# Kernel tuning notes

Measured on AMD Instinct MI355X. Metric: run time of the kernel, lower is better.

Reference implementation:

```python
import jax, jax.numpy as jnp
import numpy as np

# dims: batch, time, d_model, d_state, experts, top-k, expert hidden, regime, layers
B, T, D, S, E, K, H, R, L = 4, 512, 384, 32, 6, 2, 512, 5, 2
DI = 2 * D          # d_inner = expand * d_model
DTR = D // 16       # dt_rank = 24


def setup_inputs() -> dict:
    key = jax.random.key(0)
    ks = iter(jax.random.split(key, 48))
    def nrm(shape, s=0.02):
        return jax.random.normal(next(ks), shape, jnp.float32) * s
    inp = {}
    inp["x"] = jax.random.normal(next(ks), (B, T, D), jnp.float32)
    r = jax.random.uniform(next(ks), (B, R), jnp.float32)
    inp["regime"] = r / r.sum(-1, keepdims=True)  # regime posterior
    # FiLM conditioner
    inp["film_w1"] = nrm((R, D)); inp["film_b1"] = jnp.zeros((D,), jnp.float32)
    inp["film_w2"] = nrm((D, 2 * D)); inp["film_b2"] = jnp.zeros((2 * D,), jnp.float32)
    # SelectiveSSMBlock params, stacked over L layers
    inp["ssm_ng"] = jnp.ones((L, D), jnp.float32); inp["ssm_nb"] = jnp.zeros((L, D), jnp.float32)
    inp["in_w"] = nrm((L, D, 2 * DI))
    inp["xp_w"] = nrm((L, DI, DTR + 2 * S))
    inp["dt_w"] = nrm((L, DTR, DI)); inp["dt_b"] = jnp.zeros((L, DI), jnp.float32)
    inp["a_log_real"] = jnp.log(jnp.clip(-0.5 * jax.random.normal(next(ks), (L, DI, S), jnp.float32), 1e-4, None))
    inp["a_imag"] = 0.1 * jax.random.normal(next(ks), (L, DI, S), jnp.float32)
    inp["ssm_d"] = jnp.ones((L, DI), jnp.float32)
    inp["out_w"] = nrm((L, DI, D))
    # MoELayer params, stacked over L layers
    inp["moe_ng"] = jnp.ones((L, D), jnp.float32); inp["moe_nb"] = jnp.zeros((L, D), jnp.float32)
    inp["r_w1"] = nrm((L, D + R, D)); inp["r_b1"] = jnp.zeros((L, D), jnp.float32)
    inp["r_w2"] = nrm((L, D, E)); inp["r_b2"] = jnp.zeros((L, E), jnp.float32)
    inp["e_w1"] = nrm((L, E, D, H)); inp["e_b1"] = jnp.zeros((L, E, H), jnp.float32)
    inp["e_w2"] = nrm((L, E, H, D)); inp["e_b2"] = jnp.zeros((L, E, D), jnp.float32)
    # final norm
    inp["fin_g"] = jnp.ones((D,), jnp.float32); inp["fin_b"] = jnp.zeros((D,), jnp.float32)
    return inp


def _ln(x, g, b):
    m = x.mean(-1, keepdims=True)
    v = ((x - m) ** 2).mean(-1, keepdims=True)
    return (x - m) * jax.lax.rsqrt(v + 1e-5) * g + b


def _ssm_block(h, ng, nb, in_w, xp_w, dt_w, dt_b, alr, aim, d_vec, out_w):
    B_, T_, _ = h.shape
    xn = _ln(h, ng, nb)
    xz = xn @ in_w                        # (B,T,2*DI)
    x_ssm, z = xz[..., :DI], xz[..., DI:]
    x_dbl = x_ssm @ xp_w                  # (B,T,DTR+2S)
    dt = jax.nn.softplus(x_dbl[..., :DTR] @ dt_w + dt_b)   # (B,T,DI)
    Bp = x_dbl[..., DTR:DTR + S]          # (B,T,S)
    Cp = x_dbl[..., DTR + S:]             # (B,T,S)
    A = (-jnp.exp(alr) + 1j * aim).astype(jnp.complex64)   # (DI,S)

    def step(hc, inp):
        dt_t, bt, ct, xt = inp            # (B,DI),(B,S),(B,S),(B,DI)
        dA = jnp.exp(A[None] * dt_t[:, :, None])                       # (B,DI,S) complex
        hc = dA * hc + ((dt_t * xt)[:, :, None] * bt[:, None, :]).astype(jnp.complex64)
        # (h*C).sum(-1).real == (h.real*C).sum(-1) since C is real
        y = jnp.einsum('bds,bs->bd', hc.real, ct)
        return hc, y

    h0 = jnp.zeros((B_, DI, S), jnp.complex64)
    xsT = (jnp.moveaxis(dt, 1, 0), jnp.moveaxis(Bp, 1, 0),
           jnp.moveaxis(Cp, 1, 0), jnp.moveaxis(x_ssm, 1, 0))
    _, ysT = jax.lax.scan(step, h0, xsT)
    y = jnp.moveaxis(ysT, 0, 1) + d_vec * x_ssm   # skip term D*x
    y = y * jax.nn.silu(z)
    return h + y @ out_w                  # residual (dropout=0)


def _moe(h, regime, ng, nb, rw1, rb1, rw2, rb2, ew1, eb1, ew2, eb2):
    xn = _ln(h, ng, nb)
    B_, T_, _ = xn.shape
    reg = jnp.broadcast_to(regime[:, None, :], (B_, T_, R))
    ri = jnp.concatenate([xn, reg], -1)
    gl = jax.nn.silu(ri @ rw1 + rb1) @ rw2 + rb2    # (B,T,E)
    tv, ti = jax.lax.top_k(gl, K)
    tw = jax.nn.softmax(tv, -1)
    eo = jax.nn.silu(jnp.einsum('btd,edh->bteh', xn, ew1) + eb1)
    eo = jnp.einsum('bteh,ehd->bted', eo, ew2) + eb2   # (B,T,E,D)
    sel = jnp.take_along_axis(eo, ti[..., None], axis=2)  # (B,T,K,D)
    out = (sel * tw[..., None]).sum(2)
    gp = jax.nn.softmax(gl, -1)
    avg_p = gp.mean((0, 1))
    avg_m = jax.nn.one_hot(ti[..., 0], E, dtype=gl.dtype).mean((0, 1))
    aux = 0.01 * E * (avg_p * avg_m).sum()
    return h + out, aux


def reference(x, regime, film_w1, film_b1, film_w2, film_b2, ssm_ng, ssm_nb, in_w,
              xp_w, dt_w, dt_b, a_log_real, a_imag, ssm_d, out_w, moe_ng, moe_nb,
              r_w1, r_b1, r_w2, r_b2, e_w1, e_b1, e_w2, e_b2, fin_g, fin_b):
    # FiLM conditioning from regime posterior
    gb = jax.nn.silu(regime @ film_w1 + film_b1) @ film_w2 + film_b2
    gamma, beta = gb[:, :D], gb[:, D:]
    h = x * (gamma[:, None, :] + 1.0) + beta[:, None, :]
    aux = jnp.float32(0.0)
    for l in range(L):
        h = _ssm_block(h, ssm_ng[l], ssm_nb[l], in_w[l], xp_w[l], dt_w[l], dt_b[l],
                       a_log_real[l], a_imag[l], ssm_d[l], out_w[l])
        h, a = _moe(h, regime, moe_ng[l], moe_nb[l], r_w1[l], r_b1[l], r_w2[l], r_b2[l],
                    e_w1[l], e_b1[l], e_w2[l], e_b2[l])
        aux = aux + a
    out = _ln(h, fin_g, fin_b)
    return out, aux
```

## Files before the change

### kernel.cpp

```cpp
#include <hip/hip_runtime.h>
#include <hip/hip_bf16.h>
#include <math.h>

#define B_   4
#define T_   512
#define D_   384
#define S_   32
#define E_   6
#define H_   512
#define R_   5
#define L_   2
#define DI_  768
#define DTR_ 24
#define BT_  2048
#define XPN_ 88
#define SCH  64
#define PIT  40
#define SPD  12
#define SPB  66

typedef short s8v __attribute__((ext_vector_type(8)));
typedef float f32x4 __attribute__((ext_vector_type(4)));
typedef ushort u16x8 __attribute__((ext_vector_type(8)));

__device__ __forceinline__ float siluf(float x) { return x / (1.f + __expf(-x)); }
__device__ __forceinline__ ushort f2b(float f) {
    unsigned u = __float_as_uint(f);
    return (ushort)((u + 0x7FFFu + ((u >> 16) & 1u)) >> 16);
}
__device__ __forceinline__ float b2f(ushort h) { return __uint_as_float(((unsigned)h) << 16); }

#define CN0 1179648L
#define CN1 135168L
#define CN2 36864L
#define CN3 589824L
#define CN4 2359296L
#define CN5 2359296L
#define CN6 294912L
__global__ void conv_k(const float* __restrict__ in_w, const float* __restrict__ xp_w,
                       const float* __restrict__ dt_w, const float* __restrict__ out_w,
                       const float* __restrict__ e_w1, const float* __restrict__ e_w2,
                       const float* __restrict__ r_w1,
                       ushort* __restrict__ in_wb, ushort* __restrict__ xp_wb,
                       ushort* __restrict__ dt_wb, ushort* __restrict__ out_wb,
                       ushort* __restrict__ e1b, ushort* __restrict__ e2b,
                       ushort* __restrict__ r1h, ushort* __restrict__ r1l)
{
    const long total = CN0 + CN1 + CN2 + CN3 + CN4 + CN5 + CN6;
    long stride = (long)gridDim.x * 256;
    for (long i = (long)blockIdx.x * 256 + threadIdx.x; i < total; i += stride) {
        long j = i;
        if (j < CN0) { in_wb[j] = f2b(in_w[j]); continue; }
        j -= CN0;
        if (j < CN1) { xp_wb[j] = f2b(xp_w[j]); continue; }
        j -= CN1;
        if (j < CN2) { dt_wb[j] = f2b(dt_w[j]); continue; }
        j -= CN2;
        if (j < CN3) { out_wb[j] = f2b(out_w[j]); continue; }
        j -= CN3;
        if (j < CN4) { e1b[j] = f2b(e_w1[j]); continue; }
        j -= CN4;
        if (j < CN5) { e2b[j] = f2b(e_w2[j]); continue; }
        j -= CN5;
        {
            long l = j / 147456, rem = j - l * 147456;
            float v = r_w1[l * (long)((D_ + R_) * D_) + rem];
            ushort hv = f2b(v);
            r1h[j] = hv;
            r1l[j] = f2b(v - b2f(hv));
        }
    }
}

__global__ void film_k(const float* __restrict__ regime, const float* __restrict__ w1,
                       const float* __restrict__ b1, const float* __restrict__ w2,
                       const float* __restrict__ b2, float* __restrict__ gb,
                       float* __restrict__ stats)
{
    int b = blockIdx.x;
    int tid = threadIdx.x;
    if (b == 0 && tid < 40) stats[tid] = 0.f;
    __shared__ float t1[D_];
    if (tid < D_) {
        float a = b1[tid];
        for (int r = 0; r < R_; r++) a += regime[b * R_ + r] * w1[r * D_ + tid];
        t1[tid] = siluf(a);
    }
    __syncthreads();
    float a = b2[tid];
    for (int d = 0; d < D_; d++) a += t1[d] * w2[d * (2 * D_) + tid];
    gb[b * (2 * D_) + tid] = a;
}

__global__ void film_apply_k(const float* __restrict__ x, const float* __restrict__ gb,
                             float* __restrict__ h)
{
    int i = blockIdx.x * 256 + threadIdx.x;
    if (i >= B_ * T_ * D_) return;
    int b = i / (T_ * D_);
    int d = i % D_;
    h[i] = x[i] * (1.f + gb[b * (2 * D_) + d]) + gb[b * (2 * D_) + D_ + d];
}

template<int MODE>
__global__ __launch_bounds__(256) void ln_k(const float* __restrict__ in,
                                            const float* __restrict__ g, const float* __restrict__ b,
                                            float* __restrict__ outF,
                                            ushort* __restrict__ outH, ushort* __restrict__ outL)
{
    int row = blockIdx.x;
    int tid = threadIdx.x;
    const float* x = in + (size_t)row * D_;
    float v0 = x[tid];
    float v1 = (tid < D_ - 256) ? x[256 + tid] : 0.f;
    float s = v0 + v1, ss = v0 * v0 + v1 * v1;
#pragma unroll
    for (int o = 32; o > 0; o >>= 1) { s += __shfl_xor(s, o); ss += __shfl_xor(ss, o); }
    __shared__ float sb[8];
    int w = tid >> 6;
    if ((tid & 63) == 0) { sb[w] = s; sb[4 + w] = ss; }
    __syncthreads();
    s = sb[0] + sb[1] + sb[2] + sb[3];
    ss = sb[4] + sb[5] + sb[6] + sb[7];
    float mean = s * (1.f / D_);
    float var = ss * (1.f / D_) - mean * mean;
    float rstd = rsqrtf(var + 1e-5f);
#pragma unroll
    for (int p = 0; p < 2; p++) {
        int c = tid + p * 256;
        if (c >= D_) break;
        float v = (p ? v1 : v0);
        float o = (v - mean) * rstd * g[c] + b[c];
        size_t idx = (size_t)row * D_ + c;
        if (MODE == 0) outF[idx] = o;
        else {
            ushort hv = f2b(o);
            outH[idx] = hv;
            if (MODE == 2) outL[idx] = f2b(o - b2f(hv));
        }
    }
}

template<int MODE>
__global__ __launch_bounds__(256) void selln_k(float* __restrict__ h,
                                               const ushort* __restrict__ eodb,
                                               const float* __restrict__ tw,
                                               const int* __restrict__ tpos,
                                               const float* __restrict__ g, const float* __restrict__ b,
                                               float* __restrict__ outF,
                                               ushort* __restrict__ outH, ushort* __restrict__ outL)
{
    int row = blockIdx.x;
    int tid = threadIdx.x;
    float* hp = h + (size_t)row * D_;
    int p0 = tpos[row * 2], p1 = tpos[row * 2 + 1];
    float w0 = tw[row * 2], w1 = tw[row * 2 + 1];
    const ushort* e0 = eodb + (size_t)p0 * D_;
    const ushort* e1 = eodb + (size_t)p1 * D_;
    float v0 = hp[tid] + w0 * b2f(e0[tid]) + w1 * b2f(e1[tid]);
    float v1 = 0.f;
    if (tid < D_ - 256) v1 = hp[256 + tid] + w0 * b2f(e0[256 + tid]) + w1 * b2f(e1[256 + tid]);
    hp[tid] = v0;
    if (tid < D_ - 256) hp[256 + tid] = v1;
    float s = v0 + v1, ss = v0 * v0 + v1 * v1;
#pragma unroll
    for (int o = 32; o > 0; o >>= 1) { s += __shfl_xor(s, o); ss += __shfl_xor(ss, o); }
    __shared__ float sb[8];
    int w = tid >> 6;
    if ((tid & 63) == 0) { sb[w] = s; sb[4 + w] = ss; }
    __syncthreads();
    s = sb[0] + sb[1] + sb[2] + sb[3];
    ss = sb[4] + sb[5] + sb[6] + sb[7];
    float mean = s * (1.f / D_);
    float var = ss * (1.f / D_) - mean * mean;
    float rstd = rsqrtf(var + 1e-5f);
#pragma unroll
    for (int p = 0; p < 2; p++) {
        int c = tid + p * 256;
        if (c >= D_) break;
        float v = (p ? v1 : v0);
        float o = (v - mean) * rstd * g[c] + b[c];
        size_t idx = (size_t)row * D_ + c;
        if (MODE == 0) outF[idx] = o;
        else {
            ushort hv = f2b(o);
            outH[idx] = hv;
            if (MODE == 2) outL[idx] = f2b(o - b2f(hv));
        }
    }
}

template<int OM, bool NG, bool KG, bool GATHER>
__global__ __launch_bounds__(256) void gemm_b(
    const ushort* __restrict__ A, int lda, long aOff,
    const ushort* __restrict__ W, int ldw, long wOff,
    float* __restrict__ C, int ldc, long cOff,
    ushort* __restrict__ Cb, int ldcb, long cbOff, int nb16,
    const float* __restrict__ bias, long bOff,
    const int* __restrict__ glist, const int* __restrict__ gcnt,
    int N, int K, int act, int acc)
{
    __shared__ __align__(16) ushort As[2][64 * PIT];
    __shared__ __align__(16) ushort Bs[2][64 * PIT];
    const int z = blockIdx.z;
    const int bm = blockIdx.y * 64, bn = blockIdx.x * 64;
    int cnt = 0;
    if (gcnt) { cnt = gcnt[z]; if (bm >= cnt) return; }
    const int tid = threadIdx.x, w = tid >> 6, lane = tid & 63;
    const int wm = (w >> 1) * 32, wn = (w & 1) * 32;
    const int l16 = lane & 15, lk = lane >> 4;
    const int r0 = tid >> 2, c0 = (tid & 3) * 8;
    const ushort* Ab;
    if (GATHER) {
        int gr = bm + r0;
        int t_idx = (gr < cnt) ? glist[(size_t)z * BT_ + gr] : 0;
        Ab = A + (size_t)t_idx * lda;
    } else {
        Ab = A + (size_t)z * aOff + (size_t)(bm + r0) * lda;
    }
    const ushort* Wb = W + (size_t)z * wOff;

    f32x4 accv[2][2];
#pragma unroll
    for (int i = 0; i < 2; i++)
#pragma unroll
        for (int j = 0; j < 2; j++) accv[i][j] = (f32x4)0.f;

    u16x8 arg;
    ushort wrg[8];
    auto LOADA = [&](int k0) {
        arg = *reinterpret_cast<const u16x8*>(Ab + k0 + c0);
    };
    auto LOADW = [&](int k0) {
#pragma unroll
        for (int i = 0; i < 8; i++) {
            int kk = k0 + w * 8 + i;
            bool ok = (!KG || kk < K) && (!NG || (bn + lane) < N);
            wrg[i] = ok ? Wb[(size_t)kk * ldw + bn + lane] : (ushort)0;
        }
    };
    auto STORE = [&](int buf) {
        *reinterpret_cast<u16x8*>(&As[buf][r0 * PIT + c0]) = arg;
        *reinterpret_cast<ushort4*>(&Bs[buf][lane * PIT + w * 8]) =
            make_ushort4(wrg[0], wrg[1], wrg[2], wrg[3]);
        *reinterpret_cast<ushort4*>(&Bs[buf][lane * PIT + w * 8 + 4]) =
            make_ushort4(wrg[4], wrg[5], wrg[6], wrg[7]);
    };

    LOADA(0); LOADW(0); STORE(0);
    __syncthreads();
    const int NIT = (K + 31) / 32;
    for (int it = 0; it < NIT; it++) {
        int cur = it & 1;
        bool more = (it + 1 < NIT);
        if (more) { LOADA((it + 1) * 32); LOADW((it + 1) * 32); }
        s8v af[2], bfr[2];
#pragma unroll
        for (int mf = 0; mf < 2; mf++)
            af[mf] = *reinterpret_cast<const s8v*>(&As[cur][(wm + mf * 16 + l16) * PIT + lk * 8]);
#pragma unroll
        for (int nf = 0; nf < 2; nf++)
            bfr[nf] = *reinterpret_cast<const s8v*>(&Bs[cur][(wn + nf * 16 + l16) * PIT + lk * 8]);
#pragma unroll
        for (int mf = 0; mf < 2; mf++)
#pragma unroll
            for (int nf = 0; nf < 2; nf++)
                accv[mf][nf] = __builtin_amdgcn_mfma_f32_16x16x32_bf16(af[mf], bfr[nf], accv[mf][nf], 0, 0, 0);
        if (more) { STORE(cur ^ 1); __syncthreads(); }
    }

    const float* biasb = bias ? bias + (size_t)z * bOff : nullptr;
#pragma unroll
    for (int mf = 0; mf < 2; mf++) {
#pragma unroll
        for (int nf = 0; nf < 2; nf++) {
            int col = bn + wn + nf * 16 + l16;
            if (NG && col >= N) continue;
#pragma unroll
            for (int r = 0; r < 4; r++) {
                int rr = bm + wm + mf * 16 + lk * 4 + r;
                if (gcnt && rr >= cnt) continue;
                float v = accv[mf][nf][r];
                if (biasb) v += biasb[col];
                if (act == 1) v = siluf(v);
                else if (act == 2) v = (v > 0.f) ? v + log1pf(__expf(-v)) : log1pf(__expf(v));
                if (OM == 0 || OM == 2) {
                    float* Cz = C + (size_t)z * cOff;
                    size_t ci = (size_t)rr * ldc + col;
                    Cz[ci] = acc ? (Cz[ci] + v) : v;
                }
                if (OM == 1 || OM == 2) {
                    if (col < nb16)
                        (Cb + (size_t)z * cbOff)[(size_t)rr * ldcb + col] = f2b(v);
                }
                if (OM == 3) {
                    if (col < nb16)
                        Cb[(size_t)rr * ldcb + col] = f2b(v);
                    if (col >= 24) {
                        int q = col - 24;
                        C[(size_t)rr * 64 + ((q < 32) ? (2 * q) : (2 * (q - 32) + 1))] = v;
                    }
                }
            }
        }
    }
}

__global__ __launch_bounds__(256) void gemm3_k(
    const ushort* __restrict__ Ah, const ushort* __restrict__ Al, int lda,
    const ushort* __restrict__ Wh, const ushort* __restrict__ Wl, int ldw,
    const float* __restrict__ bias,
    const float* __restrict__ regime, const float* __restrict__ rw1t,
    const float* __restrict__ rw2l,
    float* __restrict__ glp,
    int K)
{
    __shared__ __align__(16) ushort sAh[64 * PIT], sAl[64 * PIT];
    __shared__ __align__(16) ushort sWh[64 * PIT], sWl[64 * PIT];
    __shared__ __align__(16) float sV[64 * 66];
    const int bm = blockIdx.y * 64, bn = blockIdx.x * 64;
    const int tid = threadIdx.x, w = tid >> 6, lane = tid & 63;
    const int wm = (w >> 1) * 32, wn = (w & 1) * 32;
    const int l16 = lane & 15, lk = lane >> 4;
    const int r0 = tid >> 2, c0 = (tid & 3) * 8;
    f32x4 accv[2][2];
#pragma unroll
    for (int i = 0; i < 2; i++)
#pragma unroll
        for (int j = 0; j < 2; j++) accv[i][j] = (f32x4)0.f;

    for (int k0 = 0; k0 < K; k0 += 32) {
        *reinterpret_cast<u16x8*>(&sAh[r0 * PIT + c0]) =
            *reinterpret_cast<const u16x8*>(Ah + (size_t)(bm + r0) * lda + k0 + c0);
        *reinterpret_cast<u16x8*>(&sAl[r0 * PIT + c0]) =
            *reinterpret_cast<const u16x8*>(Al + (size_t)(bm + r0) * lda + k0 + c0);
        {
            ushort th[8], tl[8];
#pragma unroll
            for (int i = 0; i < 8; i++) {
                int kk = k0 + w * 8 + i;
                th[i] = Wh[(size_t)kk * ldw + bn + lane];
                tl[i] = Wl[(size_t)kk * ldw + bn + lane];
            }
            *reinterpret_cast<ushort4*>(&sWh[lane * PIT + w * 8])     = make_ushort4(th[0], th[1], th[2], th[3]);
            *reinterpret_cast<ushort4*>(&sWh[lane * PIT + w * 8 + 4]) = make_ushort4(th[4], th[5], th[6], th[7]);
            *reinterpret_cast<ushort4*>(&sWl[lane * PIT + w * 8])     = make_ushort4(tl[0], tl[1], tl[2], tl[3]);
            *reinterpret_cast<ushort4*>(&sWl[lane * PIT + w * 8 + 4]) = make_ushort4(tl[4], tl[5], tl[6], tl[7]);
        }
        __syncthreads();
        s8v ah[2], al[2], bh[2], bl[2];
#pragma unroll
        for (int mf = 0; mf < 2; mf++) {
            ah[mf] = *reinterpret_cast<const s8v*>(&sAh[(wm + mf * 16 + l16) * PIT + lk * 8]);
            al[mf] = *reinterpret_cast<const s8v*>(&sAl[(wm + mf * 16 + l16) * PIT + lk * 8]);
        }
#pragma unroll
        for (int nf = 0; nf < 2; nf++) {
            bh[nf] = *reinterpret_cast<const s8v*>(&sWh[(wn + nf * 16 + l16) * PIT + lk * 8]);
            bl[nf] = *reinterpret_cast<const s8v*>(&sWl[(wn + nf * 16 + l16) * PIT + lk * 8]);
        }
#pragma unroll
        for (int mf = 0; mf < 2; mf++)
#pragma unroll
            for (int nf = 0; nf < 2; nf++) {
                accv[mf][nf] = __builtin_amdgcn_mfma_f32_16x16x32_bf16(ah[mf], bh[nf], accv[mf][nf], 0, 0, 0);
                accv[mf][nf] = __builtin_amdgcn_mfma_f32_16x16x32_bf16(ah[mf], bl[nf], accv[mf][nf], 0, 0, 0);
                accv[mf][nf] = __builtin_amdgcn_mfma_f32_16x16x32_bf16(al[mf], bh[nf], accv[mf][nf], 0, 0, 0);
            }
        __syncthreads();
    }
    const float* rg = regime + (bm / T_) * R_;
#pragma unroll
    for (int nf = 0; nf < 2; nf++) {
        int col = bn + wn + nf * 16 + l16;
        float rb = bias[col - bn + bn];
#pragma unroll
        for (int r = 0; r < R_; r++) rb += rg[r] * rw1t[r * D_ + col];
#pragma unroll
        for (int mf = 0; mf < 2; mf++)
#pragma unroll
            for (int r = 0; r < 4; r++) {
                int rr = wm + mf * 16 + lk * 4 + r;
                sV[rr * 66 + (col - bn)] = siluf(accv[mf][nf][r] + rb);
            }
    }
    __syncthreads();
    for (int job = tid; job < 64 * E_; job += 256) {
        int row = job / E_, e = job - row * E_;
        float a = 0.f;
#pragma unroll 8
        for (int c = 0; c < 64; c++)
            a += sV[row * 66 + c] * rw2l[(size_t)(bn + c) * E_ + e];
        glp[(size_t)blockIdx.x * (BT_ * E_) + (size_t)(bm + row) * E_ + e] = a;
    }
}

__global__ __launch_bounds__(128) void scan_k(
    const float* __restrict__ xz, const ushort* __restrict__ xdblb,
    const float* __restrict__ bcint,
    const float* __restrict__ dt_w, const float* __restrict__ dt_b,
    const float* __restrict__ alr, const float* __restrict__ aim,
    const float* __restrict__ dvecp, ushort* __restrict__ ygb)
{
    int p = blockIdx.x;
    int blk = (p & 7) * 96 + (p >> 3);
    int b = blk / 192;
    int dbase = (blk % 192) * 4;
    int tid = threadIdx.x;
    int ch = tid >> 5;
    int s = tid & 31;
    int d = dbase + ch;
    __shared__ __align__(16) float sdx[64 * SPD];
    __shared__ __align__(16) float sbc[64 * SPB];
    __shared__ float sacc[SCH * 4][33];
    int cch = tid & 3;
    float wdt[24];
#pragma unroll
    for (int k = 0; k < 24; k++) wdt[k] = dt_w[k * DI_ + dbase + cch];
    float dtbias = dt_b[dbase + cch];

    float negA = -__expf(alr[d * S_ + s]);
    float aimv = aim[d * S_ + s];
    float4 dv4 = *reinterpret_cast<const float4*>(dvecp + dbase);
    float dvc[4] = {dv4.x, dv4.y, dv4.z, dv4.w};
    float hre = 0.f, him = 0.f;
    const float* xzp = xz + (size_t)b * T_ * (2 * DI_);
    const ushort* xdp = xdblb + (size_t)b * T_ * 32;
    const float* bcp = bcint + (size_t)b * T_ * 64;
    ushort* ygp = ygb + (size_t)b * T_ * DI_;

    for (int c = 0; c < T_ / SCH; c++) {
        int tc = c * SCH;
        __syncthreads();
        if (tid < 64) {
            int t = tid;
            float4 x4 = *reinterpret_cast<const float4*>(xzp + (size_t)(tc + t) * (2 * DI_) + dbase);
            float4 z4 = *reinterpret_cast<const float4*>(xzp + (size_t)(tc + t) * (2 * DI_) + DI_ + dbase);
            sdx[t * SPD + 1] = x4.x;
            sdx[t * SPD + 3] = x4.y;
            sdx[t * SPD + 5] = x4.z;
            sdx[t * SPD + 7] = x4.w;
            sdx[t * SPD + 8]  = z4.x;
            sdx[t * SPD + 9]  = z4.y;
            sdx[t * SPD + 10] = z4.z;
            sdx[t * SPD + 11] = z4.w;
        }
        {
            int t0 = tid >> 2;
#pragma unroll
            for (int j = 0; j < 2; j++) {
                int t = t0 + j * 32;
                const ushort* xr = xdp + (size_t)(tc + t) * 32;
                u16x8 a0 = *reinterpret_cast<const u16x8*>(xr);
                u16x8 a1 = *reinterpret_cast<const u16x8*>(xr + 8);
                u16x8 a2 = *reinterpret_cast<const u16x8*>(xr + 16);
                float acc = dtbias;
#pragma unroll
                for (int k = 0; k < 8; k++) acc = fmaf(b2f((ushort)a0[k]), wdt[k], acc);
#pragma unroll
                for (int k = 0; k < 8; k++) acc = fmaf(b2f((ushort)a1[k]), wdt[8 + k], acc);
#pragma unroll
                for (int k = 0; k < 8; k++) acc = fmaf(b2f((ushort)a2[k]), wdt[16 + k], acc);
                float dtv = (acc > 0.f) ? acc + log1pf(__expf(-acc)) : log1pf(__expf(acc));
                sdx[t * SPD + 2 * cch] = dtv;
            }
        }
#pragma unroll
        for (int i = 0; i < 8; i++) {
            int idx = tid + i * 128;
            int tt = idx >> 4, q = idx & 15;
            *reinterpret_cast<float4*>(&sbc[tt * SPB + 4 * q]) =
                *reinterpret_cast<const float4*>(bcp + (size_t)(tc + tt) * 64 + 4 * q);
        }
        __syncthreads();

        const float* dxr = &sdx[2 * ch];
        const float* bcr = &sbc[2 * s];
        float2 dx0 = *reinterpret_cast<const float2*>(dxr);
        float2 bc0 = *reinterpret_cast<const float2*>(bcr);
        float2 dx1 = *reinterpret_cast<const float2*>(dxr + SPD);
        float2 bc1 = *reinterpret_cast<const float2*>(bcr + SPB);
#pragma unroll 4
        for (int t = 0; t < SCH; t++) {
            float2 dx2 = make_float2(0.f, 0.f), bc2 = dx2;
            if (t + 2 < SCH) {
                dx2 = *reinterpret_cast<const float2*>(dxr + (t + 2) * SPD);
                bc2 = *reinterpret_cast<const float2*>(bcr + (t + 2) * SPB);
            }
            float e = __expf(negA * dx0.x);
            float sn, cs;
            __sincosf(aimv * dx0.x, &sn, &cs);
            float dre = e * cs, dim = e * sn;
            float u = dx0.x * dx0.y * bc0.x;
            float nre = fmaf(dre, hre, fmaf(-dim, him, u));
            him = fmaf(dre, him, dim * hre);
            hre = nre;
            sacc[t * 4 + ch][s] = hre * bc0.y;
            dx0 = dx1; bc0 = bc1; dx1 = dx2; bc1 = bc2;
        }
        __syncthreads();

#pragma unroll
        for (int p2 = 0; p2 < 2; p2++) {
            int r = tid + p2 * 128;
            int t = r >> 2, c4 = r & 3;
            float acc = 0.f;
#pragma unroll
            for (int s2 = 0; s2 < 32; s2++) acc += sacc[r][s2];
            float xv = sdx[t * SPD + 2 * c4 + 1];
            float zv = sdx[t * SPD + 8 + c4];
            float y = (acc + dvc[c4] * xv) * siluf(zv);
            ygp[(size_t)(tc + t) * DI_ + dbase + c4] = f2b(y);
        }
    }
}

__global__ __launch_bounds__(1024) void router_assign_k(const float* __restrict__ glp,
                                                        const float* __restrict__ rb2l,
                                                        float* __restrict__ tw,
                                                        int* __restrict__ glist,
                                                        int* __restrict__ tpos,
                                                        int* __restrict__ cnt,
                                                        float* __restrict__ statL)
{
    __shared__ float s_p[E_], s_c[E_];
    __shared__ int scnt[E_];
    int tid = threadIdx.x;
    if (tid < E_) { s_p[tid] = 0.f; s_c[tid] = 0.f; scnt[tid] = 0; }
    __syncthreads();
    float lp[E_] = {0.f, 0.f, 0.f, 0.f, 0.f, 0.f};
    float lc[E_] = {0.f, 0.f, 0.f, 0.f, 0.f, 0.f};
    for (int t = tid; t < BT_; t += 1024) {
        float g[E_];
        for (int e = 0; e < E_; e++) {
            float a = rb2l[e];
#pragma unroll
            for (int j = 0; j < 6; j++) a += glp[(size_t)j * (BT_ * E_) + t * E_ + e];
            g[e] = a;
        }
        int i0 = 0; float v0 = g[0];
        for (int e = 1; e < E_; e++) if (g[e] > v0) { v0 = g[e]; i0 = e; }
        int i1 = -1; float v1 = -1e30f;
        for (int e = 0; e < E_; e++) if (e != i0 && g[e] > v1) { v1 = g[e]; i1 = e; }
        if (i1 < 0) i1 = (i0 == 0) ? 1 : 0;
        float e1 = __expf(v1 - v0);
        float inv = 1.f / (1.f + e1);
        tw[t * 2] = inv; tw[t * 2 + 1] = e1 * inv;
        int pos0 = atomicAdd(&scnt[i0], 1);
        glist[i0 * BT_ + pos0] = t;
        tpos[2 * t] = i0 * BT_ + pos0;
        int pos1 = atomicAdd(&scnt[i1], 1);
        glist[i1 * BT_ + pos1] = t;
        tpos[2 * t + 1] = i1 * BT_ + pos1;
        float pb[E_], se = 0.f;
        for (int e = 0; e < E_; e++) { pb[e] = __expf(g[e] - v0); se += pb[e]; }
        float rse = 1.f / se;
#pragma unroll
        for (int e = 0; e < E_; e++) {
            lp[e] += pb[e] * rse;
            lc[e] += (i0 == e) ? 1.f : 0.f;
        }
    }
#pragma unroll
    for (int e = 0; e < E_; e++) {
        float v = lp[e], u = lc[e];
#pragma unroll
        for (int o = 32; o > 0; o >>= 1) { v += __shfl_xor(v, o); u += __shfl_xor(u, o); }
        if ((tid & 63) == 0) { atomicAdd(&s_p[e], v); atomicAdd(&s_c[e], u); }
    }
    __syncthreads();
    if (tid < E_) {
        cnt[tid] = scnt[tid];
        statL[tid] = s_p[tid];
        statL[8 + tid] = s_c[tid];
    }
}

__global__ void write_aux_k(const float* __restrict__ stats, float* __restrict__ out)
{
    if (threadIdx.x == 0 && blockIdx.x == 0) {
        float aux = 0.f;
        for (int l = 0; l < L_; l++) {
            float s = 0.f;
            for (int e = 0; e < E_; e++) s += stats[l * 16 + e] * stats[l * 16 + 8 + e];
            aux += 0.01f * (float)E_ * s / ((float)BT_ * (float)BT_);
        }
        out[BT_ * D_] = aux;
    }
}

extern "C" void kernel_launch(void* const* d_in, const int* in_sizes, int n_in,
                              void* d_out, int out_size, void* d_ws, size_t ws_size,
                              hipStream_t stream)
{
    const float* x       = (const float*)d_in[0];
    const float* regime  = (const float*)d_in[1];
    const float* film_w1 = (const float*)d_in[2];
    const float* film_b1 = (const float*)d_in[3];
    const float* film_w2 = (const float*)d_in[4];
    const float* film_b2 = (const float*)d_in[5];
    const float* ssm_ng  = (const float*)d_in[6];
    const float* ssm_nb  = (const float*)d_in[7];
    const float* in_w    = (const float*)d_in[8];
    const float* xp_w    = (const float*)d_in[9];
    const float* dt_w    = (const float*)d_in[10];
    const float* dt_b    = (const float*)d_in[11];
    const float* alr     = (const float*)d_in[12];
    const float* aimp    = (const float*)d_in[13];
    const float* ssm_d   = (const float*)d_in[14];
    const float* out_w   = (const float*)d_in[15];
    const float* moe_ng  = (const float*)d_in[16];
    const float* moe_nb  = (const float*)d_in[17];
    const float* r_w1    = (const float*)d_in[18];
    const float* r_b1    = (const float*)d_in[19];
    const float* r_w2    = (const float*)d_in[20];
    const float* r_b2    = (const float*)d_in[21];
    const float* e_w1    = (const float*)d_in[22];
    const float* e_b1    = (const float*)d_in[23];
    const float* e_w2    = (const float*)d_in[24];
    const float* e_b2    = (const float*)d_in[25];
    const float* fin_g   = (const float*)d_in[26];
    const float* fin_b   = (const float*)d_in[27];

    float* ws = (float*)d_ws;
    size_t o = 0;
    float*  h      = ws + o; o += 786432;
    float*  stats  = ws + o; o += 64;
    ushort* xnH    = (ushort*)(ws + o); o += 393216;
    ushort* xnL    = (ushort*)(ws + o); o += 393216;
    float*  glp    = ws + o; o += 73728;
    float*  tw     = ws + o; o += 4096;
    int*    glist  = (int*)(ws + o); o += 12288;
    int*    tpos   = (int*)(ws + o); o += 4096;
    int*    cnt    = (int*)(ws + o); o += 16;
    ushort* in_wb  = (ushort*)(ws + o); o += 589824;
    ushort* xp_wb  = (ushort*)(ws + o); o += 67584;
    ushort* dt_wb  = (ushort*)(ws + o); o += 18432;
    ushort* out_wb = (ushort*)(ws + o); o += 294912;
    ushort* e1b    = (ushort*)(ws + o); o += 1179648;
    ushort* e2b    = (ushort*)(ws + o); o += 1179648;
    ushort* r1h    = (ushort*)(ws + o); o += 147456;
    ushort* r1l    = (ushort*)(ws + o); o += 147456;
    float*  xz    = ws + o;
    ushort* xzb   = (ushort*)(ws + o + 3145728);
    ushort* xdblb = (ushort*)(ws + o + 3932160);
    float*  bcint = ws + o + 3964928;
    ushort* ygb   = (ushort*)(ws + o + 4096000);
    ushort* eohb  = (ushort*)(ws + o + 786432);
    ushort* eodb  = (ushort*)(ws + o + 3932160);
    float*  gb    = ws + o;

    conv_k<<<2048, 256, 0, stream>>>(in_w, xp_w, dt_w, out_w, e_w1, e_w2, r_w1,
                                     in_wb, xp_wb, dt_wb, out_wb, e1b, e2b, r1h, r1l);
    film_k<<<B_, 2 * D_, 0, stream>>>(regime, film_w1, film_b1, film_w2, film_b2, gb, stats);
    film_apply_k<<<(B_ * T_ * D_ + 255) / 256, 256, 0, stream>>>(x, gb, h);

    for (int l = 0; l < L_; l++) {
        if (l == 0)
            ln_k<1><<<BT_, 256, 0, stream>>>(h, ssm_ng, ssm_nb, nullptr, xnH, nullptr);
        gemm_b<2, false, false, false><<<dim3(24, 32), 256, 0, stream>>>(
            xnH, D_, 0, in_wb + (size_t)l * 589824, 2 * DI_, 0,
            xz, 2 * DI_, 0, xzb, DI_, 0, DI_,
            nullptr, 0, nullptr, nullptr, 2 * DI_, D_, 0, 0);
        gemm_b<3, true, false, false><<<dim3(2, 32), 256, 0, stream>>>(
            xzb, DI_, 0, xp_wb + (size_t)l * 67584, XPN_, 0,
            bcint, 64, 0, xdblb, 32, 0, 32,
            nullptr, 0, nullptr, nullptr, XPN_, DI_, 0, 0);
        scan_k<<<B_ * 192, 128, 0, stream>>>(
            xz, xdblb, bcint,
            dt_w + (size_t)l * DTR_ * DI_, dt_b + l * DI_,
            alr + (size_t)l * DI_ * S_, aimp + (size_t)l * DI_ * S_,
            ssm_d + l * DI_, ygb);
        gemm_b<0, false, false, false><<<dim3(6, 32), 256, 0, stream>>>(
            ygb, DI_, 0, out_wb + (size_t)l * 294912, D_, 0,
            h, D_, 0, nullptr, 0, 0, 0,
            nullptr, 0, nullptr, nullptr, D_, DI_, 0, 1);

        ln_k<2><<<BT_, 256, 0, stream>>>(h, moe_ng + l * D_, moe_nb + l * D_, nullptr, xnH, xnL);
        gemm3_k<<<dim3(6, 32), 256, 0, stream>>>(
            xnH, xnL, D_, r1h + (size_t)l * 147456, r1l + (size_t)l * 147456, D_,
            r_b1 + l * D_,
            regime, r_w1 + (size_t)l * ((D_ + R_) * D_) + (size_t)D_ * D_,
            r_w2 + (size_t)l * D_ * E_,
            glp, D_);
        router_assign_k<<<1, 1024, 0, stream>>>(glp, r_b2 + l * E_, tw, glist, tpos, cnt, stats + l * 16);
        gemm_b<1, false, false, true><<<dim3(8, 32, 6), 256, 0, stream>>>(
            xnH, D_, 0, e1b + (size_t)l * 1179648, H_, (long)D_ * H_,
            nullptr, 0, 0, eohb, H_, (long)BT_ * H_, H_,
            e_b1 + (size_t)l * E_ * H_, H_, glist, cnt, H_, D_, 1, 0);
        gemm_b<1, false, false, false><<<dim3(6, 32, 6), 256, 0, stream>>>(
            eohb, H_, (long)BT_ * H_, e2b + (size_t)l * 1179648, D_, (long)H_ * D_,
            nullptr, 0, 0, eodb, D_, (long)BT_ * D_, D_,
            e_b2 + (size_t)l * E_ * D_, D_, nullptr, cnt, D_, H_, 0, 0);
        if (l < L_ - 1)
            selln_k<1><<<BT_, 256, 0, stream>>>(h, eodb, tw, tpos,
                ssm_ng + (l + 1) * D_, ssm_nb + (l + 1) * D_, nullptr, xnH, nullptr);
        else
            selln_k<0><<<BT_, 256, 0, stream>>>(h, eodb, tw, tpos,
                fin_g, fin_b, (float*)d_out, nullptr, nullptr);
    }

    write_aux_k<<<1, 64, 0, stream>>>(stats, (float*)d_out);
}
```

Baseline: 478.2 us.

## Fuse FiLM apply with first LayerNorm, fold aux write, drop unused dt_w conversion

Merges the FiLM affine application and the first layer's LayerNorm into one row kernel, so h is not written and then reread. The aux-loss computation moves into the final selln kernel, which removes a separate launch. Conversion of dt_w to bf16 is dropped because the scan reads dt_w in fp32. The scan loop's shared-memory prefetch depth grows from two steps to three, which adds registers.

```diff
diff --git a/kernel.cpp b/kernel.cpp
--- a/kernel.cpp
+++ b/kernel.cpp
@@ -32,21 +32,20 @@
 
 #define CN0 1179648L
 #define CN1 135168L
-#define CN2 36864L
 #define CN3 589824L
 #define CN4 2359296L
 #define CN5 2359296L
 #define CN6 294912L
 __global__ void conv_k(const float* __restrict__ in_w, const float* __restrict__ xp_w,
-                       const float* __restrict__ dt_w, const float* __restrict__ out_w,
+                       const float* __restrict__ out_w,
                        const float* __restrict__ e_w1, const float* __restrict__ e_w2,
                        const float* __restrict__ r_w1,
                        ushort* __restrict__ in_wb, ushort* __restrict__ xp_wb,
-                       ushort* __restrict__ dt_wb, ushort* __restrict__ out_wb,
+                       ushort* __restrict__ out_wb,
                        ushort* __restrict__ e1b, ushort* __restrict__ e2b,
                        ushort* __restrict__ r1h, ushort* __restrict__ r1l)
 {
-    const long total = CN0 + CN1 + CN2 + CN3 + CN4 + CN5 + CN6;
+    const long total = CN0 + CN1 + CN3 + CN4 + CN5 + CN6;
     long stride = (long)gridDim.x * 256;
     for (long i = (long)blockIdx.x * 256 + threadIdx.x; i < total; i += stride) {
         long j = i;
@@ -54,8 +53,6 @@
         j -= CN0;
         if (j < CN1) { xp_wb[j] = f2b(xp_w[j]); continue; }
         j -= CN1;
-        if (j < CN2) { dt_wb[j] = f2b(dt_w[j]); continue; }
-        j -= CN2;
         if (j < CN3) { out_wb[j] = f2b(out_w[j]); continue; }
         j -= CN3;
         if (j < CN4) { e1b[j] = f2b(e_w1[j]); continue; }
@@ -92,14 +89,38 @@
     gb[b * (2 * D_) + tid] = a;
 }
 
-__global__ void film_apply_k(const float* __restrict__ x, const float* __restrict__ gb,
-                             float* __restrict__ h)
-{
-    int i = blockIdx.x * 256 + threadIdx.x;
-    if (i >= B_ * T_ * D_) return;
-    int b = i / (T_ * D_);
-    int d = i % D_;
-    h[i] = x[i] * (1.f + gb[b * (2 * D_) + d]) + gb[b * (2 * D_) + D_ + d];
+__global__ __launch_bounds__(256) void film_ln_k(const float* __restrict__ x,
+                                                 const float* __restrict__ gb,
+                                                 float* __restrict__ h,
+                                                 const float* __restrict__ g, const float* __restrict__ b,
+                                                 ushort* __restrict__ outH)
+{
+    int row = blockIdx.x;
+    int tid = threadIdx.x;
+    int bb = row / T_;
+    const float* xp = x + (size_t)row * D_;
+    const float* gbp = gb + bb * (2 * D_);
+    float v0 = xp[tid] * (1.f + gbp[tid]) + gbp[D_ + tid];
+    float v1 = 0.f;
+    if (tid < D_ - 256) v1 = xp[256 + tid] * (1.f + gbp[256 + tid]) + gbp[D_ + 256 + tid];
+    float* hp = h + (size_t)row * D_;
+    hp[tid] = v0;
+    if (tid < D_ - 256) hp[256 + tid] = v1;
+    float s = v0 + v1, ss = v0 * v0 + v1 * v1;
+#pragma unroll
+    for (int o = 32; o > 0; o >>= 1) { s += __shfl_xor(s, o); ss += __shfl_xor(ss, o); }
+    __shared__ float sb[8];
+    int w = tid >> 6;
+    if ((tid & 63) == 0) { sb[w] = s; sb[4 + w] = ss; }
+    __syncthreads();
+    s = sb[0] + sb[1] + sb[2] + sb[3];
+    ss = sb[4] + sb[5] + sb[6] + sb[7];
+    float mean = s * (1.f / D_);
+    float var = ss * (1.f / D_) - mean * mean;
+    float rstd = rsqrtf(var + 1e-5f);
+    outH[(size_t)row * D_ + tid] = f2b((v0 - mean) * rstd * g[tid] + b[tid]);
+    if (tid < D_ - 256)
+        outH[(size_t)row * D_ + 256 + tid] = f2b((v1 - mean) * rstd * g[256 + tid] + b[256 + tid]);
 }
 
 template<int MODE>
@@ -148,10 +169,20 @@
                                                const int* __restrict__ tpos,
                                                const float* __restrict__ g, const float* __restrict__ b,
                                                float* __restrict__ outF,
-                                               ushort* __restrict__ outH, ushort* __restrict__ outL)
+                                               ushort* __restrict__ outH, ushort* __restrict__ outL,
+                                               const float* __restrict__ stats)
 {
     int row = blockIdx.x;
     int tid = threadIdx.x;
+    if (MODE == 0 && row == 0 && tid == 0) {
+        float aux = 0.f;
+        for (int l = 0; l < L_; l++) {
+            float s2 = 0.f;
+            for (int e = 0; e < E_; e++) s2 += stats[l * 16 + e] * stats[l * 16 + 8 + e];
+            aux += 0.01f * (float)E_ * s2 / ((float)BT_ * (float)BT_);
+        }
+        outF[BT_ * D_] = aux;
+    }
     float* hp = h + (size_t)row * D_;
     int p0 = tpos[row * 2], p1 = tpos[row * 2 + 1];
     float w0 = tw[row * 2], w1 = tw[row * 2 + 1];
@@ -373,7 +404,7 @@
 #pragma unroll
     for (int nf = 0; nf < 2; nf++) {
         int col = bn + wn + nf * 16 + l16;
-        float rb = bias[col - bn + bn];
+        float rb = bias[col];
 #pragma unroll
         for (int r = 0; r < R_; r++) rb += rg[r] * rw1t[r * D_ + col];
 #pragma unroll
@@ -476,27 +507,31 @@
 
         const float* dxr = &sdx[2 * ch];
         const float* bcr = &sbc[2 * s];
-        float2 dx0 = *reinterpret_cast<const float2*>(dxr);
-        float2 bc0 = *reinterpret_cast<const float2*>(bcr);
-        float2 dx1 = *reinterpret_cast<const float2*>(dxr + SPD);
-        float2 bc1 = *reinterpret_cast<const float2*>(bcr + SPB);
+        float2 dxa = *reinterpret_cast<const float2*>(dxr);
+        float2 bca = *reinterpret_cast<const float2*>(bcr);
+        float2 dxb = *reinterpret_cast<const float2*>(dxr + SPD);
+        float2 bcb = *reinterpret_cast<const float2*>(bcr + SPB);
+        float2 dxc = *reinterpret_cast<const float2*>(dxr + 2 * SPD);
+        float2 bcc = *reinterpret_cast<const float2*>(bcr + 2 * SPB);
 #pragma unroll 4
         for (int t = 0; t < SCH; t++) {
-            float2 dx2 = make_float2(0.f, 0.f), bc2 = dx2;
-            if (t + 2 < SCH) {
-                dx2 = *reinterpret_cast<const float2*>(dxr + (t + 2) * SPD);
-                bc2 = *reinterpret_cast<const float2*>(bcr + (t + 2) * SPB);
+            float2 dxn = make_float2(0.f, 0.f), bcn = dxn;
+            if (t + 3 < SCH) {
+                dxn = *reinterpret_cast<const float2*>(dxr + (t + 3) * SPD);
+                bcn = *reinterpret_cast<const float2*>(bcr + (t + 3) * SPB);
             }
-            float e = __expf(negA * dx0.x);
+            float e = __expf(negA * dxa.x);
             float sn, cs;
-            __sincosf(aimv * dx0.x, &sn, &cs);
+            __sincosf(aimv * dxa.x, &sn, &cs);
             float dre = e * cs, dim = e * sn;
-            float u = dx0.x * dx0.y * bc0.x;
+            float u = dxa.x * dxa.y * bca.x;
             float nre = fmaf(dre, hre, fmaf(-dim, him, u));
             him = fmaf(dre, him, dim * hre);
             hre = nre;
-            sacc[t * 4 + ch][s] = hre * bc0.y;
-            dx0 = dx1; bc0 = bc1; dx1 = dx2; bc1 = bc2;
+            sacc[t * 4 + ch][s] = hre * bca.y;
+            dxa = dxb; bca = bcb;
+            dxb = dxc; bcb = bcc;
+            dxc = dxn; bcc = bcn;
         }
         __syncthreads();
 
@@ -573,19 +608,6 @@
         cnt[tid] = scnt[tid];
         statL[tid] = s_p[tid];
         statL[8 + tid] = s_c[tid];
-    }
-}
-
-__global__ void write_aux_k(const float* __restrict__ stats, float* __restrict__ out)
-{
-    if (threadIdx.x == 0 && blockIdx.x == 0) {
-        float aux = 0.f;
-        for (int l = 0; l < L_; l++) {
-            float s = 0.f;
-            for (int e = 0; e < E_; e++) s += stats[l * 16 + e] * stats[l * 16 + 8 + e];
-            aux += 0.01f * (float)E_ * s / ((float)BT_ * (float)BT_);
-        }
-        out[BT_ * D_] = aux;
     }
 }
 
@@ -635,7 +657,6 @@
     int*    cnt    = (int*)(ws + o); o += 16;
     ushort* in_wb  = (ushort*)(ws + o); o += 589824;
     ushort* xp_wb  = (ushort*)(ws + o); o += 67584;
-    ushort* dt_wb  = (ushort*)(ws + o); o += 18432;
     ushort* out_wb = (ushort*)(ws + o); o += 294912;
     ushort* e1b    = (ushort*)(ws + o); o += 1179648;
     ushort* e2b    = (ushort*)(ws + o); o += 1179648;
@@ -650,14 +671,12 @@
     ushort* eodb  = (ushort*)(ws + o + 3932160);
     float*  gb    = ws + o;
 
-    conv_k<<<2048, 256, 0, stream>>>(in_w, xp_w, dt_w, out_w, e_w1, e_w2, r_w1,
-                                     in_wb, xp_wb, dt_wb, out_wb, e1b, e2b, r1h, r1l);
+    conv_k<<<2048, 256, 0, stream>>>(in_w, xp_w, out_w, e_w1, e_w2, r_w1,
+                                     in_wb, xp_wb, out_wb, e1b, e2b, r1h, r1l);
     film_k<<<B_, 2 * D_, 0, stream>>>(regime, film_w1, film_b1, film_w2, film_b2, gb, stats);
-    film_apply_k<<<(B_ * T_ * D_ + 255) / 256, 256, 0, stream>>>(x, gb, h);
+    film_ln_k<<<BT_, 256, 0, stream>>>(x, gb, h, ssm_ng, ssm_nb, xnH);
 
     for (int l = 0; l < L_; l++) {
-        if (l == 0)
-            ln_k<1><<<BT_, 256, 0, stream>>>(h, ssm_ng, ssm_nb, nullptr, xnH, nullptr);
         gemm_b<2, false, false, false><<<dim3(24, 32), 256, 0, stream>>>(
             xnH, D_, 0, in_wb + (size_t)l * 589824, 2 * DI_, 0,
             xz, 2 * DI_, 0, xzb, DI_, 0, DI_,
@@ -694,11 +713,9 @@
             e_b2 + (size_t)l * E_ * D_, D_, nullptr, cnt, D_, H_, 0, 0);
         if (l < L_ - 1)
             selln_k<1><<<BT_, 256, 0, stream>>>(h, eodb, tw, tpos,
-                ssm_ng + (l + 1) * D_, ssm_nb + (l + 1) * D_, nullptr, xnH, nullptr);
+                ssm_ng + (l + 1) * D_, ssm_nb + (l + 1) * D_, nullptr, xnH, nullptr, nullptr);
         else
             selln_k<0><<<BT_, 256, 0, stream>>>(h, eodb, tw, tpos,
-                fin_g, fin_b, (float*)d_out, nullptr, nullptr);
-    }
-
-    write_aux_k<<<1, 64, 0, stream>>>(stats, (float*)d_out);
-}
+                fin_g, fin_b, (float*)d_out, nullptr, nullptr, stats);
+    }
+}
```

Result: no change. 472.5 us (-1.2%).
